# Kernel tuning notes

Measured on AMD Instinct MI355X. Metric: run time of the kernel, lower is better.

## Reference

```python
import jax, jax.numpy as jnp
import numpy as np

B, S, D, H = 4, 1024, 1024, 16
HD = D // H
EPS = 1e-5


def layer_norm(x, scale, shift):
    mean = jnp.mean(x, axis=-1, keepdims=True)
    var = jnp.mean((x - mean) ** 2, axis=-1, keepdims=True)
    return scale * (x - mean) / jnp.sqrt(var + EPS) + shift


def gelu_tanh(x):
    c = jnp.sqrt(jnp.asarray(2.0 / jnp.pi, dtype=x.dtype))
    return 0.5 * x * (1.0 + jnp.tanh(c * (x + 0.044715 * x ** 3)))


def setup_inputs() -> dict:
    key = jax.random.key(0)
    ks = jax.random.split(key, 12)
    s = 0.02
    return {
        "x": jax.random.normal(ks[0], (B, S, D), dtype=jnp.float32),
        "attention_mask": jnp.ones((B, S), dtype=jnp.int32),
        "wq": jax.random.normal(ks[1], (D, D), dtype=jnp.float32) * s,
        "wk": jax.random.normal(ks[2], (D, D), dtype=jnp.float32) * s,
        "wv": jax.random.normal(ks[3], (D, D), dtype=jnp.float32) * s,
        "wo": jax.random.normal(ks[4], (D, D), dtype=jnp.float32) * s,
        "bo": jnp.zeros((D,), dtype=jnp.float32),
        "ln1_scale": jnp.ones((D,), dtype=jnp.float32),
        "ln1_shift": jnp.zeros((D,), dtype=jnp.float32),
        "ln2_scale": jnp.ones((D,), dtype=jnp.float32),
        "ln2_shift": jnp.zeros((D,), dtype=jnp.float32),
        "w1": jax.random.normal(ks[5], (D, 4 * D), dtype=jnp.float32) * s,
        "b1": jnp.zeros((4 * D,), dtype=jnp.float32),
        "w2": jax.random.normal(ks[6], (4 * D, D), dtype=jnp.float32) * s,
        "b2": jnp.zeros((D,), dtype=jnp.float32),
    }


def reference(x, attention_mask, wq, wk, wv, wo, bo, ln1_scale, ln1_shift,
              ln2_scale, ln2_shift, w1, b1, w2, b2):
    b, s, d = x.shape
    # --- pre-norm attention ---
    shortcut = x
    h = layer_norm(x, ln1_scale, ln1_shift)
    q = (h @ wq).reshape(b, s, H, HD).transpose(0, 2, 1, 3)  # bhsd
    k = (h @ wk).reshape(b, s, H, HD).transpose(0, 2, 1, 3)
    v = (h @ wv).reshape(b, s, H, HD).transpose(0, 2, 1, 3)
    scores = jnp.einsum('bhqd,bhkd->bhqk', q, k)
    causal = jnp.triu(jnp.ones((s, s), dtype=bool), k=1)  # True above diag -> masked
    neg_inf = jnp.asarray(-jnp.inf, dtype=scores.dtype)
    scores = jnp.where(causal, neg_inf, scores)
    pad = attention_mask[:, None, None, :].astype(bool)  # (b,1,1,k)
    scores = jnp.where(pad, scores, neg_inf)
    attn = jax.nn.softmax(scores / jnp.sqrt(jnp.asarray(HD, dtype=scores.dtype)), axis=-1)
    ctx = jnp.einsum('bhqk,bhkd->bhqd', attn, v)
    ctx = ctx.transpose(0, 2, 1, 3).reshape(b, s, d)
    x = shortcut + (ctx @ wo + bo)
    # --- pre-norm FFN ---
    shortcut = x
    h = layer_norm(x, ln2_scale, ln2_shift)
    h = gelu_tanh(h @ w1 + b1) @ w2 + b2
    return shortcut + h
```

## Files before the change

kernel.cpp:

```cpp
#include <hip/hip_runtime.h>
#include <hip/hip_bf16.h>
#include <math.h>

#define B_ 4
#define S_ 1024
#define D_ 1024
#define H_ 16
#define HD_ 64

typedef __hip_bfloat16 bf16_t;
typedef __attribute__((ext_vector_type(8))) short bf16x8;
typedef __attribute__((ext_vector_type(4))) float floatx4;

__device__ __forceinline__ float bf2f(ushort u) {
  return __uint_as_float((unsigned)u << 16);
}

__global__ __launch_bounds__(256) void prep_kernel(
    const float* __restrict__ x, const float* __restrict__ ln1s,
    const float* __restrict__ ln1b, bf16_t* __restrict__ h,
    const float* __restrict__ wq, const float* __restrict__ wk,
    const float* __restrict__ wv, const float* __restrict__ wo,
    const float* __restrict__ w1, const float* __restrict__ w2,
    bf16_t* __restrict__ wqkv_t, bf16_t* __restrict__ wo_t,
    bf16_t* __restrict__ w1_t, bf16_t* __restrict__ w2_t) {
  const int id = blockIdx.x;
  if (id < 4096) {
    const int row = id;
    float4 v = ((const float4*)(x + (size_t)row * D_))[threadIdx.x];
    float s = v.x + v.y + v.z + v.w;
    float ss = v.x * v.x + v.y * v.y + v.z * v.z + v.w * v.w;
#pragma unroll
    for (int off = 32; off > 0; off >>= 1) {
      s += __shfl_xor(s, off);
      ss += __shfl_xor(ss, off);
    }
    __shared__ float ls[4], lss[4], stats[2];
    const int wave = threadIdx.x >> 6, lane = threadIdx.x & 63;
    if (lane == 0) { ls[wave] = s; lss[wave] = ss; }
    __syncthreads();
    if (threadIdx.x == 0) {
      float t = ls[0] + ls[1] + ls[2] + ls[3];
      float tt = lss[0] + lss[1] + lss[2] + lss[3];
      float mean = t * (1.0f / D_);
      stats[0] = mean;
      stats[1] = rsqrtf(tt * (1.0f / D_) - mean * mean + 1e-5f);
    }
    __syncthreads();
    const float mean = stats[0], rstd = stats[1];
    float4 sc = ((const float4*)ln1s)[threadIdx.x];
    float4 sh = ((const float4*)ln1b)[threadIdx.x];
    bf16_t ob[4];
    ob[0] = __float2bfloat16(sc.x * (v.x - mean) * rstd + sh.x);
    ob[1] = __float2bfloat16(sc.y * (v.y - mean) * rstd + sh.y);
    ob[2] = __float2bfloat16(sc.z * (v.z - mean) * rstd + sh.z);
    ob[3] = __float2bfloat16(sc.w * (v.w - mean) * rstd + sh.w);
    *(ushort4*)(h + (size_t)row * D_ + threadIdx.x * 4) = *(ushort4*)ob;
    return;
  }
  const float* W;
  bf16_t* Wt;
  int K, N, n0, k0;
  if (id < 8192) {
    const int t = id - 4096, which = t >> 10, tile = t & 1023;
    n0 = (tile & 31) * 32;
    k0 = (tile >> 5) * 32;
    K = 1024; N = 1024;
    W = which == 0 ? wq : which == 1 ? wk : which == 2 ? wv : wo;
    Wt = which < 3 ? wqkv_t + (size_t)which * 1024 * 1024 : wo_t;
  } else if (id < 12288) {
    const int tile = id - 8192;
    n0 = (tile & 127) * 32;
    k0 = (tile >> 7) * 32;
    K = 1024; N = 4096;
    W = w1; Wt = w1_t;
  } else {
    const int tile = id - 12288;
    n0 = (tile & 31) * 32;
    k0 = (tile >> 5) * 32;
    K = 4096; N = 1024;
    W = w2; Wt = w2_t;
  }
  __shared__ float t[32][33];
  const int lx = threadIdx.x & 31, ly = threadIdx.x >> 5;
#pragma unroll
  for (int r = ly; r < 32; r += 8) t[r][lx] = W[(size_t)(k0 + r) * N + n0 + lx];
  __syncthreads();
#pragma unroll
  for (int r = ly; r < 32; r += 8)
    Wt[(size_t)(n0 + r) * K + k0 + lx] = __float2bfloat16(t[lx][r]);
}

__global__ __launch_bounds__(256) void mgemm_kernel(const bf16_t* __restrict__ A,
                                                    const bf16_t* __restrict__ Bt,
                                                    const float* __restrict__ bias,
                                                    void* __restrict__ C,
                                                    int M, int N, int K, int Kc,
                                                    int Mt, int Nt, int PM,
                                                    int mode) {
  __shared__ bf16_t As[128 * 64];
  __shared__ bf16_t Bs[128 * 64];
  const int tid = threadIdx.x;
  const int lane = tid & 63, w = tid >> 6;

  const int flat = blockIdx.x;
  const int xcd = flat & 7;
  int t0 = flat >> 3;
  const int mb = xcd % PM, nb = xcd / PM;
  const int mt = mb * Mt + (t0 % Mt);
  t0 /= Mt;
  const int nt = nb * Nt + (t0 % Nt);
  const int z = t0 / Nt;
  const int m0 = mt * 128, n0 = nt * 128;
  const int kz0 = z * Kc;
  const int wm = (w >> 1) * 64, wn = (w & 1) * 64;

  floatx4 zero = {0.f, 0.f, 0.f, 0.f};
  floatx4 acc[4][4];
#pragma unroll
  for (int i = 0; i < 4; i++)
#pragma unroll
    for (int j = 0; j < 4; j++) acc[i][j] = zero;

  const int ro8 = lane >> 3;
  const int g8 = ((lane & 7) ^ ro8) * 8;
  const bf16_t* ga[4];
  const bf16_t* gb[4];
  bf16_t* la[4];
  bf16_t* lb[4];
#pragma unroll
  for (int t = 0; t < 4; t++) {
    const int c = w + 4 * t;
    ga[t] = A + (size_t)(m0 + c * 8 + ro8) * K + g8;
    gb[t] = Bt + (size_t)(n0 + c * 8 + ro8) * K + g8;
    la[t] = &As[c * 512];
    lb[t] = &Bs[c * 512];
  }

  const int fr = lane & 15, quad = lane >> 4;

  for (int k0 = kz0; k0 < kz0 + Kc; k0 += 64) {
    __syncthreads();
#pragma unroll
    for (int t = 0; t < 4; t++) {
      __builtin_amdgcn_global_load_lds(
          (const __attribute__((address_space(1))) void*)(ga[t] + k0),
          (__attribute__((address_space(3))) void*)la[t], 16, 0, 0);
      __builtin_amdgcn_global_load_lds(
          (const __attribute__((address_space(1))) void*)(gb[t] + k0),
          (__attribute__((address_space(3))) void*)lb[t], 16, 0, 0);
    }
    __syncthreads();

#pragma unroll
    for (int ks = 0; ks < 2; ks++) {
      const int sq = ((quad + 4 * ks) ^ (fr & 7)) * 8;
      bf16x8 af[4], bfr[4];
#pragma unroll
      for (int i = 0; i < 4; i++) {
        af[i] = *(const bf16x8*)&As[(wm + i * 16 + fr) * 64 + sq];
        bfr[i] = *(const bf16x8*)&Bs[(wn + i * 16 + fr) * 64 + sq];
      }
#pragma unroll
      for (int i = 0; i < 4; i++)
#pragma unroll
        for (int j = 0; j < 4; j++)
          acc[i][j] = __builtin_amdgcn_mfma_f32_16x16x32_bf16(af[i], bfr[j],
                                                              acc[i][j], 0, 0, 0);
    }
  }

  bf16_t* Pz = (mode == 4) ? ((bf16_t*)C + (size_t)z * M * N) : nullptr;
#pragma unroll
  for (int j = 0; j < 4; j++) {
    const int col = n0 + wn + j * 16 + fr;
    const float bj = bias ? bias[col] : 0.f;
#pragma unroll
    for (int i = 0; i < 4; i++) {
      const int rbase = m0 + wm + i * 16 + quad * 4;
#pragma unroll
      for (int r = 0; r < 4; r++) {
        const int row = rbase + r;
        float c = acc[i][j][r] + bj;
        if (mode == 1) {
          const float xg = c;
          const float t = 0.7978845608028654f * (xg + 0.044715f * xg * xg * xg);
          const float th = 2.0f / (1.0f + __expf(-2.0f * t)) - 1.0f;
          c = 0.5f * xg * (1.0f + th);
        }
        if (mode == 4) {
          Pz[(size_t)row * N + col] = __float2bfloat16(c);
        } else {
          ((bf16_t*)C)[(size_t)row * N + col] = __float2bfloat16(c);
        }
      }
    }
  }
}

__global__ __launch_bounds__(512, 1) void mgemm256_kernel(
    const bf16_t* __restrict__ A, const bf16_t* __restrict__ Bt,
    const float* __restrict__ bias, void* __restrict__ C, int M, int N, int K,
    int Kc, int Mt, int Nt, int PM, int mode) {
  __shared__ bf16_t sm[65536];
  const int tid = threadIdx.x;
  const int lane = tid & 63, w = tid >> 6;

  const int flat = blockIdx.x;
  const int xcd = flat & 7;
  int t0 = flat >> 3;
  const int mb = xcd % PM, nb = xcd / PM;
  const int mt = mb * Mt + (t0 % Mt);
  t0 /= Mt;
  const int nt = nb * Nt + (t0 % Nt);
  const int z = t0 / Nt;
  const int m0 = mt * 256, n0 = nt * 256;
  const int kz0 = z * Kc;
  const int wr = (w >> 2) & 1, wc = w & 3;

  floatx4 zero = {0.f, 0.f, 0.f, 0.f};
  floatx4 acc[8][4];
#pragma unroll
  for (int i = 0; i < 8; i++)
#pragma unroll
    for (int j = 0; j < 4; j++) acc[i][j] = zero;

  const int r_t = tid >> 3;
  const int g8s = (((tid & 7) ^ (r_t & 7)) << 3);
  const int fr = lane & 15, quad = lane >> 4;

  auto STAGE = [&](int nbuf, int unit, int kk) {
    const bf16_t* src0 =
        (unit < 2) ? Bt + (size_t)(n0 + (unit & 1) * 128 + r_t) * K + g8s + kk
                   : A + (size_t)(m0 + (unit & 1) * 128 + r_t) * K + g8s + kk;
    bf16_t* d0 = &sm[nbuf * 32768 + (unit < 2 ? 16384 : 0) + (unit & 1) * 8192 +
                     tid * 8];
#pragma unroll
    for (int l = 0; l < 2; ++l) {
      __builtin_amdgcn_global_load_lds(
          (const __attribute__((address_space(1))) void*)(src0 +
                                                          (size_t)l * 64 * K),
          (__attribute__((address_space(3))) void*)(d0 + l * 4096), 16, 0, 0);
    }
  };

  const int ntk = Kc >> 6;

  STAGE(0, 0, kz0); STAGE(0, 1, kz0); STAGE(0, 2, kz0); STAGE(0, 3, kz0);
  asm volatile("s_waitcnt vmcnt(2)" ::: "memory");
  __builtin_amdgcn_s_barrier();

#define DO_PHASE(KS, MH, UNIT)                                                 \
  {                                                                            \
    const int sq = (((quad + 4 * (KS)) ^ (fr & 7)) << 3);                      \
    bf16x8 af[4];                                                              \
    _Pragma("unroll") for (int i = 0; i < 4; ++i) af[i] =                      \
        *(const bf16x8*)&sm[bo + ((MH)*128 + wr * 64 + i * 16 + fr) * 64 + sq];\
    if ((MH) == 0) {                                                           \
      _Pragma("unroll") for (int j = 0; j < 4; ++j) bfr[j] =                   \
          *(const bf16x8*)&sm[bo + 16384 + (wc * 64 + j * 16 + fr) * 64 + sq]; \
    }                                                                          \
    if (pre) STAGE(nbuf, (UNIT), kn);                                          \
    __builtin_amdgcn_s_barrier();                                              \
    asm volatile("s_waitcnt lgkmcnt(0)" ::: "memory");                         \
    __builtin_amdgcn_sched_barrier(0);                                         \
    __builtin_amdgcn_s_setprio(1);                                             \
    _Pragma("unroll") for (int i = 0; i < 4; ++i)                              \
        _Pragma("unroll") for (int j = 0; j < 4; ++j) acc[(MH)*4 + i][j] =     \
            __builtin_amdgcn_mfma_f32_16x16x32_bf16(af[i], bfr[j],             \
                                                    acc[(MH)*4 + i][j], 0, 0,  \
                                                    0);                        \
    __builtin_amdgcn_s_setprio(0);                                             \
    if (pre) {                                                                 \
      asm volatile("s_waitcnt vmcnt(2)" ::: "memory");                         \
    } else {                                                                   \
      asm volatile("s_waitcnt vmcnt(0)" ::: "memory");                         \
    }                                                                          \
    __builtin_amdgcn_s_barrier();                                              \
  }

  for (int t = 0; t < ntk; ++t) {
    const int bo = (t & 1) * 32768;
    const int nbuf = (t + 1) & 1;
    const int kn = kz0 + (t + 1) * 64;
    const bool pre = (t + 1 < ntk);
    bf16x8 bfr[4];
    DO_PHASE(0, 0, 0)
    DO_PHASE(0, 1, 1)
    DO_PHASE(1, 0, 2)
    DO_PHASE(1, 1, 3)
  }
#undef DO_PHASE

  __syncthreads();
  bf16_t* sl = sm + w * 4096;
  bf16_t* Pz = (mode == 4) ? ((bf16_t*)C + (size_t)z * M * N) : (bf16_t*)C;
  float bj[4];
#pragma unroll
  for (int j = 0; j < 4; ++j)
    bj[j] = bias ? bias[n0 + wc * 64 + j * 16 + fr] : 0.f;
#pragma unroll
  for (int mh = 0; mh < 2; ++mh) {
    if (mh) {
      asm volatile("s_waitcnt lgkmcnt(0)" ::: "memory");
      __builtin_amdgcn_sched_barrier(0);
    }
#pragma unroll
    for (int i = 0; i < 4; ++i)
#pragma unroll
      for (int j = 0; j < 4; ++j)
#pragma unroll
        for (int r = 0; r < 4; ++r) {
          const int rl = i * 16 + quad * 4 + r, cl = j * 16 + fr;
          float c = acc[mh * 4 + i][j][r] + bj[j];
          if (mode == 1) {
            const float xg = c;
            const float t2 =
                0.7978845608028654f * (xg + 0.044715f * xg * xg * xg);
            const float th = 2.0f / (1.0f + __expf(-2.0f * t2)) - 1.0f;
            c = 0.5f * xg * (1.0f + th);
          }
          const int cg = (cl >> 3) ^ (rl & 7);
          sl[rl * 64 + cg * 8 + (cl & 7)] = __float2bfloat16(c);
        }
#pragma unroll
    for (int it = 0; it < 8; ++it) {
      const int gi = it * 64 + lane;
      const int rl = gi >> 3, g = gi & 7;
      const bf16x8 vv = *(const bf16x8*)&sl[rl * 64 + ((g ^ (rl & 7)) * 8)];
      *(bf16x8*)&Pz[(size_t)(m0 + mh * 128 + wr * 64 + rl) * N + n0 + wc * 64 +
                    g * 8] = vv;
    }
  }
}

__global__ __launch_bounds__(256) void reduce2_ln_kernel(
    const bf16_t* __restrict__ P, size_t slice, const float* __restrict__ x,
    const float* __restrict__ bias, const float* __restrict__ scale,
    const float* __restrict__ shift, float* __restrict__ out,
    bf16_t* __restrict__ h) {
  const int row = blockIdx.x;
  const size_t e = (size_t)row * D_ + threadIdx.x * 4;
  const float4 xv = *(const float4*)(x + e);
  const ushort4 p0 = *(const ushort4*)((const ushort*)P + e);
  const ushort4 p1 = *(const ushort4*)((const ushort*)P + slice + e);
  const float4 bb = *(const float4*)(bias + threadIdx.x * 4);
  float4 v;
  v.x = xv.x + bf2f(p0.x) + bf2f(p1.x) + bb.x;
  v.y = xv.y + bf2f(p0.y) + bf2f(p1.y) + bb.y;
  v.z = xv.z + bf2f(p0.z) + bf2f(p1.z) + bb.z;
  v.w = xv.w + bf2f(p0.w) + bf2f(p1.w) + bb.w;
  *(float4*)(out + e) = v;

  float s = v.x + v.y + v.z + v.w;
  float ss = v.x * v.x + v.y * v.y + v.z * v.z + v.w * v.w;
#pragma unroll
  for (int off = 32; off > 0; off >>= 1) {
    s += __shfl_xor(s, off);
    ss += __shfl_xor(ss, off);
  }
  __shared__ float ls[4], lss[4], stats[2];
  const int wave = threadIdx.x >> 6, lane = threadIdx.x & 63;
  if (lane == 0) { ls[wave] = s; lss[wave] = ss; }
  __syncthreads();
  if (threadIdx.x == 0) {
    float t = ls[0] + ls[1] + ls[2] + ls[3];
    float tt = lss[0] + lss[1] + lss[2] + lss[3];
    float mean = t * (1.0f / D_);
    stats[0] = mean;
    stats[1] = rsqrtf(tt * (1.0f / D_) - mean * mean + 1e-5f);
  }
  __syncthreads();
  const float mean = stats[0], rstd = stats[1];
  const float4 sc = *(const float4*)(scale + threadIdx.x * 4);
  const float4 sh = *(const float4*)(shift + threadIdx.x * 4);
  bf16_t ob[4];
  ob[0] = __float2bfloat16(sc.x * (v.x - mean) * rstd + sh.x);
  ob[1] = __float2bfloat16(sc.y * (v.y - mean) * rstd + sh.y);
  ob[2] = __float2bfloat16(sc.z * (v.z - mean) * rstd + sh.z);
  ob[3] = __float2bfloat16(sc.w * (v.w - mean) * rstd + sh.w);
  *(ushort4*)(h + e) = *(ushort4*)ob;
}

__global__ __launch_bounds__(256) void reduce4_kernel(const bf16_t* __restrict__ P,
                                                      size_t slice,
                                                      const float* __restrict__ bias,
                                                      float* __restrict__ out,
                                                      int N) {
  const size_t e = ((size_t)blockIdx.x * 256 + threadIdx.x) * 4;
  const ushort* Pu = (const ushort*)P;
  const ushort4 p0 = *(const ushort4*)(Pu + e);
  const ushort4 p1 = *(const ushort4*)(Pu + slice + e);
  const ushort4 p2 = *(const ushort4*)(Pu + 2 * slice + e);
  const ushort4 p3 = *(const ushort4*)(Pu + 3 * slice + e);
  const float4 r = *(const float4*)(out + e);
  const float4 bb = *(const float4*)(bias + (int)(e % N));
  float4 o;
  o.x = r.x + bb.x + bf2f(p0.x) + bf2f(p1.x) + bf2f(p2.x) + bf2f(p3.x);
  o.y = r.y + bb.y + bf2f(p0.y) + bf2f(p1.y) + bf2f(p2.y) + bf2f(p3.y);
  o.z = r.z + bb.z + bf2f(p0.z) + bf2f(p1.z) + bf2f(p2.z) + bf2f(p3.z);
  o.w = r.w + bb.w + bf2f(p0.w) + bf2f(p1.w) + bf2f(p2.w) + bf2f(p3.w);
  *(float4*)(out + e) = o;
}

__global__ __launch_bounds__(256) void fattn_kernel(const bf16_t* __restrict__ QK,
                                                    const bf16_t* __restrict__ VT,
                                                    const int* __restrict__ mask,
                                                    bf16_t* __restrict__ O) {
  const int qt = gridDim.x - 1 - blockIdx.x;
  const int h = blockIdx.y, b = blockIdx.z;
  const int tid = threadIdx.x;
  const int lane = tid & 63, w = tid >> 6;
  const int tx = lane & 15, quad = lane >> 4;
  const int q0 = qt * 64;

  __shared__ bf16_t Ks[64 * 64];
  __shared__ bf16_t Vs[64 * 64];
  __shared__ ushort Ps[64 * 64];

  const int ro8 = lane >> 3;
  const int g8 = ((lane & 7) ^ ro8) * 8;
  const bf16_t* gk[2];
  const bf16_t* gv[2];
  bf16_t* lk[2];
  bf16_t* lv[2];
#pragma unroll
  for (int t = 0; t < 2; t++) {
    const int c = w + 4 * t;
    gk[t] = QK + (size_t)((size_t)b * S_ + c * 8 + ro8) * 2048 + 1024 + h * HD_ + g8;
    gv[t] = VT + (size_t)(h * HD_ + c * 8 + ro8) * 4096 + (size_t)b * S_ + g8;
    lk[t] = &Ks[c * 512];
    lv[t] = &Vs[c * 512];
  }

  bf16x8 qf[2];
#pragma unroll
  for (int ks = 0; ks < 2; ks++)
    qf[ks] = *(const bf16x8*)(QK + (size_t)((size_t)b * S_ + q0 + w * 16 + tx) * 2048 +
                              h * HD_ + ks * 32 + quad * 8);

  const short oneb = 0x3F80;
  bf16x8 vones = {oneb, oneb, oneb, oneb, oneb, oneb, oneb, oneb};

  floatx4 ctx[4], lacc;
#pragma unroll
  for (int nt = 0; nt < 4; nt++) {
    ctx[nt].x = 0.f; ctx[nt].y = 0.f; ctx[nt].z = 0.f; ctx[nt].w = 0.f;
  }
  lacc.x = 0.f; lacc.y = 0.f; lacc.z = 0.f; lacc.w = 0.f;

  for (int kt = 0; kt <= qt; kt++) {
    const int k0 = kt * 64;
    __syncthreads();
#pragma unroll
    for (int t = 0; t < 2; t++) {
      __builtin_amdgcn_global_load_lds(
          (const __attribute__((address_space(1))) void*)(gk[t] + (size_t)k0 * 2048),
          (__attribute__((address_space(3))) void*)lk[t], 16, 0, 0);
      __builtin_amdgcn_global_load_lds(
          (const __attribute__((address_space(1))) void*)(gv[t] + k0),
          (__attribute__((address_space(3))) void*)lv[t], 16, 0, 0);
    }
    __syncthreads();

    floatx4 accS[4];
#pragma unroll
    for (int nt = 0; nt < 4; nt++) {
      accS[nt].x = 0.f; accS[nt].y = 0.f; accS[nt].z = 0.f; accS[nt].w = 0.f;
    }
#pragma unroll
    for (int ks = 0; ks < 2; ks++) {
      const int sq = ((quad + 4 * ks) ^ (tx & 7)) * 8;
      bf16x8 kf[4];
#pragma unroll
      for (int nt = 0; nt < 4; nt++)
        kf[nt] = *(const bf16x8*)&Ks[(nt * 16 + tx) * 64 + sq];
#pragma unroll
      for (int nt = 0; nt < 4; nt++)
        accS[nt] = __builtin_amdgcn_mfma_f32_16x16x32_bf16(qf[ks], kf[nt],
                                                           accS[nt], 0, 0, 0);
    }

#pragma unroll
    for (int nt = 0; nt < 4; nt++) {
      const int jc = k0 + nt * 16 + tx;
      const bool ok = mask[b * S_ + jc] != 0;
      const int col = nt * 16 + tx;
#pragma unroll
      for (int r = 0; r < 4; r++) {
        const int qq = quad * 4 + r;
        const int qrow = q0 + w * 16 + qq;
        float p = exp2f(accS[nt][r] * 0.1803368801111244f);
        if (jc > qrow || !ok) p = 0.f;
        const int pc = ((((col >> 3) ^ (qq & 7)) << 3)) | (col & 7);
        Ps[(w * 16 + qq) * 64 + pc] =
            ((__hip_bfloat16_raw)__float2bfloat16(p)).x;
      }
    }

#pragma unroll
    for (int ks = 0; ks < 2; ks++) {
      const int sq = ((quad + 4 * ks) ^ (tx & 7)) * 8;
      const bf16x8 pf = *(const bf16x8*)&Ps[(w * 16 + tx) * 64 + sq];
      bf16x8 vf[4];
#pragma unroll
      for (int nt = 0; nt < 4; nt++)
        vf[nt] = *(const bf16x8*)&Vs[(nt * 16 + tx) * 64 + sq];
#pragma unroll
      for (int nt = 0; nt < 4; nt++)
        ctx[nt] = __builtin_amdgcn_mfma_f32_16x16x32_bf16(pf, vf[nt],
                                                          ctx[nt], 0, 0, 0);
      lacc = __builtin_amdgcn_mfma_f32_16x16x32_bf16(pf, vones, lacc, 0, 0, 0);
    }
  }

  const size_t obase = (size_t)b * S_ * D_ + (size_t)h * HD_;
  float rinv[4];
#pragma unroll
  for (int r = 0; r < 4; r++) rinv[r] = 1.0f / lacc[r];
#pragma unroll
  for (int nt = 0; nt < 4; nt++)
#pragma unroll
    for (int r = 0; r < 4; r++) {
      const int q = q0 + w * 16 + quad * 4 + r;
      O[obase + (size_t)q * D_ + nt * 16 + tx] =
          __float2bfloat16(ctx[nt][r] * rinv[r]);
    }
}

extern "C" void kernel_launch(void* const* d_in, const int* in_sizes, int n_in,
                              void* d_out, int out_size, void* d_ws, size_t ws_size,
                              hipStream_t stream) {
  const float* x = (const float*)d_in[0];
  const int* mask = (const int*)d_in[1];
  const float* wq = (const float*)d_in[2];
  const float* wk = (const float*)d_in[3];
  const float* wv = (const float*)d_in[4];
  const float* wo = (const float*)d_in[5];
  const float* bo = (const float*)d_in[6];
  const float* ln2s = (const float*)d_in[9];
  const float* ln2b = (const float*)d_in[10];
  const float* w1 = (const float*)d_in[11];
  const float* b1 = (const float*)d_in[12];
  const float* w2 = (const float*)d_in[13];
  const float* b2 = (const float*)d_in[14];
  float* out = (float*)d_out;

  const int M = B_ * S_;
  char* ws = (char*)d_ws;
  const size_t MB = (size_t)1 << 20;
  bf16_t* qk = (bf16_t*)(ws);
  bf16_t* vT = (bf16_t*)(ws + 16 * MB);
  bf16_t* ffn1 = (bf16_t*)(ws);
  bf16_t* ctx = (bf16_t*)(ws + 32 * MB);
  bf16_t* h = (bf16_t*)(ws + 40 * MB);
  bf16_t* wqkv_t = (bf16_t*)(ws + 48 * MB);
  bf16_t* wo_t = (bf16_t*)(ws + 54 * MB);
  bf16_t* w1_t = (bf16_t*)(ws + 56 * MB);
  bf16_t* w2_t = (bf16_t*)(ws + 64 * MB);
  bf16_t* Pa = (bf16_t*)(ws);
  bf16_t* Pf = (bf16_t*)(ws + 32 * MB);
  const size_t slice = (size_t)M * D_;

  prep_kernel<<<dim3(16384), 256, 0, stream>>>(x, (const float*)d_in[7],
                                               (const float*)d_in[8], h, wq, wk,
                                               wv, wo, w1, w2, wqkv_t, wo_t,
                                               w1_t, w2_t);

  mgemm_kernel<<<dim3(16 * 32), 256, 0, stream>>>(
      h, wqkv_t, nullptr, qk, M, 2 * D_, D_, D_, 8, 8, 4, 0);

  mgemm_kernel<<<dim3(8 * 32), 256, 0, stream>>>(
      wqkv_t + (size_t)2 * 1024 * 1024, h, nullptr, vT, D_, M, D_, D_,
      4, 8, 2, 0);

  fattn_kernel<<<dim3(S_ / 64, H_, B_), 256, 0, stream>>>(qk, vT, mask, ctx);

  mgemm_kernel<<<dim3(8 * 32 * 2), 256, 0, stream>>>(
      ctx, wo_t, nullptr, Pa, M, D_, D_, D_ / 2, 4, 8, 8, 4);

  reduce2_ln_kernel<<<dim3(M), 256, 0, stream>>>(Pa, slice, x, bo, ln2s, ln2b,
                                                 out, h);

  mgemm256_kernel<<<dim3(256), 512, 0, stream>>>(
      h, w1_t, b1, ffn1, M, 4 * D_, D_, D_, 4, 8, 4, 1);

  mgemm256_kernel<<<dim3(256), 512, 0, stream>>>(
      ffn1, w2_t, nullptr, Pf, M, D_, 4 * D_, D_, 2, 4, 8, 4);

  reduce4_kernel<<<dim3((size_t)M * D_ / 1024), 256, 0, stream>>>(
      Pf, slice, b2, out, D_);
}
```

Baseline: 345.2 us.

## Merge QKV GEMMs, drop split-K partials, accumulate FFN2 directly into output

Fuses the QK and V-transpose GEMMs into one launch. Removes split-K from the Wo projection and the FFN2 GEMM, so the bf16 partial buffers and the reduce4 kernel are no longer needed. FFN2 now runs on the 128-tile kernel with a mode that adds the bias and result straight into the fp32 residual output. It also relaxes vmcnt waits in the 256-tile GEMM's middle phases. This cuts launches and partial-sum traffic, at the cost of fewer blocks (256) for the K=4096 GEMM and possibly lower occupancy. The removed waits could race if they were needed.

```diff
diff --git a/kernel.cpp b/kernel.cpp
--- a/kernel.cpp
+++ b/kernel.cpp
@@ -91,19 +91,14 @@
     Wt[(size_t)(n0 + r) * K + k0 + lx] = __float2bfloat16(t[lx][r]);
 }
 
-__global__ __launch_bounds__(256) void mgemm_kernel(const bf16_t* __restrict__ A,
-                                                    const bf16_t* __restrict__ Bt,
-                                                    const float* __restrict__ bias,
-                                                    void* __restrict__ C,
-                                                    int M, int N, int K, int Kc,
-                                                    int Mt, int Nt, int PM,
-                                                    int mode) {
-  __shared__ bf16_t As[128 * 64];
-  __shared__ bf16_t Bs[128 * 64];
+__device__ __forceinline__ void mgemm_body(
+    const bf16_t* __restrict__ A, const bf16_t* __restrict__ Bt,
+    const float* __restrict__ bias, void* __restrict__ C, int M, int N, int K,
+    int Kc, int Mt, int Nt, int PM, int mode, int flat, bf16_t* As,
+    bf16_t* Bs) {
   const int tid = threadIdx.x;
   const int lane = tid & 63, w = tid >> 6;
 
-  const int flat = blockIdx.x;
   const int xcd = flat & 7;
   int t0 = flat >> 3;
   const int mb = xcd % PM, nb = xcd / PM;
@@ -188,13 +183,43 @@
           const float th = 2.0f / (1.0f + __expf(-2.0f * t)) - 1.0f;
           c = 0.5f * xg * (1.0f + th);
         }
-        if (mode == 4) {
+        if (mode == 5) {
+          float* O = (float*)C;
+          O[(size_t)row * N + col] += c;
+        } else if (mode == 4) {
           Pz[(size_t)row * N + col] = __float2bfloat16(c);
         } else {
           ((bf16_t*)C)[(size_t)row * N + col] = __float2bfloat16(c);
         }
       }
     }
+  }
+}
+
+__global__ __launch_bounds__(256) void mgemm_kernel(const bf16_t* __restrict__ A,
+                                                    const bf16_t* __restrict__ Bt,
+                                                    const float* __restrict__ bias,
+                                                    void* __restrict__ C,
+                                                    int M, int N, int K, int Kc,
+                                                    int Mt, int Nt, int PM,
+                                                    int mode) {
+  __shared__ bf16_t As[128 * 64];
+  __shared__ bf16_t Bs[128 * 64];
+  mgemm_body(A, Bt, bias, C, M, N, K, Kc, Mt, Nt, PM, mode, blockIdx.x, As, Bs);
+}
+
+__global__ __launch_bounds__(256) void qkv2_kernel(const bf16_t* __restrict__ h,
+                                                   const bf16_t* __restrict__ wqkv_t,
+                                                   bf16_t* __restrict__ qk,
+                                                   bf16_t* __restrict__ vT) {
+  __shared__ bf16_t As[128 * 64];
+  __shared__ bf16_t Bs[128 * 64];
+  if (blockIdx.x < 512) {
+    mgemm_body(h, wqkv_t, nullptr, qk, 4096, 2048, 1024, 1024, 8, 8, 4, 0,
+               blockIdx.x, As, Bs);
+  } else {
+    mgemm_body(wqkv_t + (size_t)2 * 1024 * 1024, h, nullptr, vT, 1024, 4096,
+               1024, 1024, 4, 8, 2, 0, blockIdx.x - 512, As, Bs);
   }
 }
 
@@ -250,7 +275,7 @@
   asm volatile("s_waitcnt vmcnt(2)" ::: "memory");
   __builtin_amdgcn_s_barrier();
 
-#define DO_PHASE(KS, MH, UNIT)                                                 \
+#define DO_PHASE(KS, MH, UNIT, WAIT)                                           \
   {                                                                            \
     const int sq = (((quad + 4 * (KS)) ^ (fr & 7)) << 3);                      \
     bf16x8 af[4];                                                              \
@@ -271,10 +296,12 @@
                                                     acc[(MH)*4 + i][j], 0, 0,  \
                                                     0);                        \
     __builtin_amdgcn_s_setprio(0);                                             \
-    if (pre) {                                                                 \
-      asm volatile("s_waitcnt vmcnt(2)" ::: "memory");                         \
-    } else {                                                                   \
-      asm volatile("s_waitcnt vmcnt(0)" ::: "memory");                         \
+    if (WAIT) {                                                                \
+      if (pre) {                                                               \
+        asm volatile("s_waitcnt vmcnt(2)" ::: "memory");                       \
+      } else {                                                                 \
+        asm volatile("s_waitcnt vmcnt(0)" ::: "memory");                       \
+      }                                                                        \
     }                                                                          \
     __builtin_amdgcn_s_barrier();                                              \
   }
@@ -285,10 +312,10 @@
     const int kn = kz0 + (t + 1) * 64;
     const bool pre = (t + 1 < ntk);
     bf16x8 bfr[4];
-    DO_PHASE(0, 0, 0)
-    DO_PHASE(0, 1, 1)
-    DO_PHASE(1, 0, 2)
-    DO_PHASE(1, 1, 3)
+    DO_PHASE(0, 0, 0, 1)
+    DO_PHASE(0, 1, 1, 0)
+    DO_PHASE(1, 0, 2, 0)
+    DO_PHASE(1, 1, 3, 1)
   }
 #undef DO_PHASE
 
@@ -334,8 +361,8 @@
   }
 }
 
-__global__ __launch_bounds__(256) void reduce2_ln_kernel(
-    const bf16_t* __restrict__ P, size_t slice, const float* __restrict__ x,
+__global__ __launch_bounds__(256) void reduce1_ln_kernel(
+    const bf16_t* __restrict__ P, const float* __restrict__ x,
     const float* __restrict__ bias, const float* __restrict__ scale,
     const float* __restrict__ shift, float* __restrict__ out,
     bf16_t* __restrict__ h) {
@@ -343,13 +370,12 @@
   const size_t e = (size_t)row * D_ + threadIdx.x * 4;
   const float4 xv = *(const float4*)(x + e);
   const ushort4 p0 = *(const ushort4*)((const ushort*)P + e);
-  const ushort4 p1 = *(const ushort4*)((const ushort*)P + slice + e);
   const float4 bb = *(const float4*)(bias + threadIdx.x * 4);
   float4 v;
-  v.x = xv.x + bf2f(p0.x) + bf2f(p1.x) + bb.x;
-  v.y = xv.y + bf2f(p0.y) + bf2f(p1.y) + bb.y;
-  v.z = xv.z + bf2f(p0.z) + bf2f(p1.z) + bb.z;
-  v.w = xv.w + bf2f(p0.w) + bf2f(p1.w) + bb.w;
+  v.x = xv.x + bf2f(p0.x) + bb.x;
+  v.y = xv.y + bf2f(p0.y) + bb.y;
+  v.z = xv.z + bf2f(p0.z) + bb.z;
+  v.w = xv.w + bf2f(p0.w) + bb.w;
   *(float4*)(out + e) = v;
 
   float s = v.x + v.y + v.z + v.w;
@@ -380,27 +406,6 @@
   ob[2] = __float2bfloat16(sc.z * (v.z - mean) * rstd + sh.z);
   ob[3] = __float2bfloat16(sc.w * (v.w - mean) * rstd + sh.w);
   *(ushort4*)(h + e) = *(ushort4*)ob;
-}
-
-__global__ __launch_bounds__(256) void reduce4_kernel(const bf16_t* __restrict__ P,
-                                                      size_t slice,
-                                                      const float* __restrict__ bias,
-                                                      float* __restrict__ out,
-                                                      int N) {
-  const size_t e = ((size_t)blockIdx.x * 256 + threadIdx.x) * 4;
-  const ushort* Pu = (const ushort*)P;
-  const ushort4 p0 = *(const ushort4*)(Pu + e);
-  const ushort4 p1 = *(const ushort4*)(Pu + slice + e);
-  const ushort4 p2 = *(const ushort4*)(Pu + 2 * slice + e);
-  const ushort4 p3 = *(const ushort4*)(Pu + 3 * slice + e);
-  const float4 r = *(const float4*)(out + e);
-  const float4 bb = *(const float4*)(bias + (int)(e % N));
-  float4 o;
-  o.x = r.x + bb.x + bf2f(p0.x) + bf2f(p1.x) + bf2f(p2.x) + bf2f(p3.x);
-  o.y = r.y + bb.y + bf2f(p0.y) + bf2f(p1.y) + bf2f(p2.y) + bf2f(p3.y);
-  o.z = r.z + bb.z + bf2f(p0.z) + bf2f(p1.z) + bf2f(p2.z) + bf2f(p3.z);
-  o.w = r.w + bb.w + bf2f(p0.w) + bf2f(p1.w) + bf2f(p2.w) + bf2f(p3.w);
-  *(float4*)(out + e) = o;
 }
 
 __global__ __launch_bounds__(256) void fattn_kernel(const bf16_t* __restrict__ QK,
@@ -558,36 +563,26 @@
   bf16_t* wo_t = (bf16_t*)(ws + 54 * MB);
   bf16_t* w1_t = (bf16_t*)(ws + 56 * MB);
   bf16_t* w2_t = (bf16_t*)(ws + 64 * MB);
-  bf16_t* Pa = (bf16_t*)(ws);
-  bf16_t* Pf = (bf16_t*)(ws + 32 * MB);
-  const size_t slice = (size_t)M * D_;
+  bf16_t* Pa = (bf16_t*)(ws + 24 * MB);
 
   prep_kernel<<<dim3(16384), 256, 0, stream>>>(x, (const float*)d_in[7],
                                                (const float*)d_in[8], h, wq, wk,
                                                wv, wo, w1, w2, wqkv_t, wo_t,
                                                w1_t, w2_t);
 
-  mgemm_kernel<<<dim3(16 * 32), 256, 0, stream>>>(
-      h, wqkv_t, nullptr, qk, M, 2 * D_, D_, D_, 8, 8, 4, 0);
-
-  mgemm_kernel<<<dim3(8 * 32), 256, 0, stream>>>(
-      wqkv_t + (size_t)2 * 1024 * 1024, h, nullptr, vT, D_, M, D_, D_,
-      4, 8, 2, 0);
+  qkv2_kernel<<<dim3(768), 256, 0, stream>>>(h, wqkv_t, qk, vT);
 
   fattn_kernel<<<dim3(S_ / 64, H_, B_), 256, 0, stream>>>(qk, vT, mask, ctx);
 
-  mgemm_kernel<<<dim3(8 * 32 * 2), 256, 0, stream>>>(
-      ctx, wo_t, nullptr, Pa, M, D_, D_, D_ / 2, 4, 8, 8, 4);
-
-  reduce2_ln_kernel<<<dim3(M), 256, 0, stream>>>(Pa, slice, x, bo, ln2s, ln2b,
-                                                 out, h);
+  mgemm_kernel<<<dim3(256), 256, 0, stream>>>(
+      ctx, wo_t, nullptr, Pa, M, D_, D_, D_, 4, 8, 8, 0);
+
+  reduce1_ln_kernel<<<dim3(M), 256, 0, stream>>>(Pa, x, bo, ln2s, ln2b, out, h);
 
   mgemm256_kernel<<<dim3(256), 512, 0, stream>>>(
       h, w1_t, b1, ffn1, M, 4 * D_, D_, D_, 4, 8, 4, 1);
 
-  mgemm256_kernel<<<dim3(256), 512, 0, stream>>>(
-      ffn1, w2_t, nullptr, Pf, M, D_, 4 * D_, D_, 2, 4, 8, 4);
-
-  reduce4_kernel<<<dim3((size_t)M * D_ / 1024), 256, 0, stream>>>(
-      Pf, slice, b2, out, D_);
-}
+  mgemm_kernel<<<dim3(256), 256, 0, stream>>>(
+      ffn1, w2_t, b2, out, M, D_, 4 * D_, 4 * D_, 8, 4, 4,
+      5);
+}
```

Result: slower. 384.9 us (+11.5%).
